# Performance work log

Measured on AMD Instinct MI355X. Metric: run time of the kernel, lower is better.

## Reference

```python
import jax, jax.numpy as jnp
import numpy as np
import math

EMBED_DIM = 128
NUM_HEADS = 8
HEAD_DIM = EMBED_DIM // NUM_HEADS
# Faithful to the source's concat bug: heads [0,1,1,2,3,4,5,6] (head 7 dropped, head 1 duplicated)
HEAD_ORDER = [0, 1, 1, 2, 3, 4, 5, 6]


def setup_inputs() -> dict:
    key = jax.random.key(0)
    ks = jax.random.split(key, 7)
    B, S = 4, 2048
    input_embeddings = jax.random.normal(ks[0], (B, S, EMBED_DIM), dtype=jnp.float32)
    token_attention_masks = jax.random.randint(ks[1], (B, S), 0, 2, dtype=jnp.int64)
    # torch.rand -> uniform [0,1)
    w_query = jax.random.uniform(ks[2], (EMBED_DIM, EMBED_DIM), dtype=jnp.float32)
    w_key = jax.random.uniform(ks[3], (EMBED_DIM, EMBED_DIM), dtype=jnp.float32)
    w_value = jax.random.uniform(ks[4], (EMBED_DIM, EMBED_DIM), dtype=jnp.float32)
    # nn.Linear params
    lim = 1.0 / math.sqrt(EMBED_DIM)
    lin_w = jax.random.uniform(ks[5], (EMBED_DIM, EMBED_DIM), dtype=jnp.float32, minval=-lim, maxval=lim)
    lin_b = jax.random.uniform(ks[6], (EMBED_DIM,), dtype=jnp.float32, minval=-lim, maxval=lim)
    return {"input_embeddings": input_embeddings, "token_attention_masks": token_attention_masks,
            "w_query": w_query, "w_key": w_key, "w_value": w_value, "lin_w": lin_w, "lin_b": lin_b}


def reference(input_embeddings, token_attention_masks, w_query, w_key, w_value, lin_w, lin_b):
    B, S, _ = input_embeddings.shape
    q = input_embeddings @ w_query  # [B,S,D]
    k = input_embeddings @ w_key
    v = input_embeddings @ w_value
    # split heads: [B,S,H,hd] -> [B,H,S,hd]
    qh = q.reshape(B, S, NUM_HEADS, HEAD_DIM).transpose(0, 2, 1, 3)
    kh = k.reshape(B, S, NUM_HEADS, HEAD_DIM).transpose(0, 2, 1, 3)
    vh = v.reshape(B, S, NUM_HEADS, HEAD_DIM).transpose(0, 2, 1, 3)
    # NOTE: source scales by sqrt(full embedding dim), not sqrt(head_dim)
    scale = 1.0 / math.sqrt(EMBED_DIM)
    scores = jnp.einsum('bhsd,bhtd->bhst', qh, kh) * scale  # [B,H,S,S]
    # mask: 0 -> -1000, 1 -> 0; broadcast over query positions
    mask = jnp.where(token_attention_masks == 0, -1000.0, 0.0).astype(scores.dtype)  # [B,S]
    scores = scores + mask[:, None, None, :]
    probs = jax.nn.softmax(scores, axis=-1)
    out_h = jnp.einsum('bhst,bhtd->bhsd', probs, vh)  # [B,H,S,hd]
    # buggy concat order kept faithful
    attn_out = jnp.concatenate([out_h[:, i] for i in HEAD_ORDER], axis=-1)  # [B,S,D]
    return attn_out @ lin_w.T + lin_b
```

## Files before the change

kernel.cpp:

```cpp
#include <hip/hip_runtime.h>
#include <stdint.h>

typedef unsigned short u16;
typedef unsigned int   u32;
typedef float   f32x4  __attribute__((ext_vector_type(4)));
typedef float   f32x16 __attribute__((ext_vector_type(16)));
typedef __bf16  bf16x8 __attribute__((ext_vector_type(8)));
typedef u32     u32x4  __attribute__((ext_vector_type(4)));
typedef u32     u32x2  __attribute__((ext_vector_type(2)));

union BF8 { bf16x8 v; u16 s[8]; u32x4 q; };

__device__ __forceinline__ u16 f2b_rne(float f) {
    u32 u = __builtin_bit_cast(u32, f);
    u32 r = u + 0x7FFFu + ((u >> 16) & 1u);
    return (u16)(r >> 16);
}
__device__ __forceinline__ u16 f2b_trunc(float f) {
    return (u16)(__builtin_bit_cast(u32, f) >> 16);
}
__device__ __forceinline__ float b2f(u16 h) {
    u32 u = ((u32)h) << 16;
    return __builtin_bit_cast(float, u);
}
__device__ __forceinline__ bf16x8 ld_bf8(const u16* p) {
    BF8 t; t.q = *(const u32x4*)p; return t.v;
}
__device__ __forceinline__ f32x16 zero16() {
    f32x16 z;
#pragma unroll
    for (int i = 0; i < 16; i++) z[i] = 0.f;
    return z;
}
__device__ __forceinline__ f32x4 zero4() {
    f32x4 z;
#pragma unroll
    for (int i = 0; i < 4; i++) z[i] = 0.f;
    return z;
}

#define SCALE2 0.1275312959479341f
#define MBIAS2 -1442.6950408889634f

__global__ __launch_bounds__(256) void proj_kernel(
    const float* __restrict__ x, const float* __restrict__ wq,
    const float* __restrict__ wk, const float* __restrict__ wv,
    u16* Qph, u16* Qpl, u16* Kph, u16* Kpl, u16* VT)
{
    int typ  = blockIdx.y;
    int ct   = threadIdx.x >> 6;
    int lane = threadIdx.x & 63;
    int m = lane & 31, kg = lane >> 5;
    int r0 = blockIdx.x * 32;
    int c = ct * 32 + m;

    const float* wp = (typ == 0) ? wq : (typ == 1) ? wk : wv;

    f32x16 acc = zero16();
#pragma unroll 4
    for (int kk = 0; kk < 128; kk += 16) {
        const float* xp = x + (size_t)(r0 + m) * 128 + kk + kg * 8;
        f32x4 x0 = *(const f32x4*)xp;
        f32x4 x1 = *(const f32x4*)(xp + 4);
        BF8 ah, al;
#pragma unroll
        for (int j = 0; j < 4; j++) {
            u16 hb = f2b_trunc(x0[j]);
            ah.s[j] = hb; al.s[j] = f2b_trunc(x0[j] - b2f(hb));
            u16 hb2 = f2b_trunc(x1[j]);
            ah.s[4 + j] = hb2; al.s[4 + j] = f2b_trunc(x1[j] - b2f(hb2));
        }
        const float* wcol = wp + (size_t)(kk + kg * 8) * 128 + c;
        if (typ < 2) {
            BF8 bh, bl_;
#pragma unroll
            for (int j = 0; j < 8; j++) {
                float w = wcol[(size_t)j * 128];
                u16 hb = f2b_trunc(w);
                bh.s[j] = hb; bl_.s[j] = f2b_trunc(w - b2f(hb));
            }
            acc = __builtin_amdgcn_mfma_f32_32x32x16_bf16(ah.v, bh.v, acc, 0, 0, 0);
            acc = __builtin_amdgcn_mfma_f32_32x32x16_bf16(ah.v, bl_.v, acc, 0, 0, 0);
            acc = __builtin_amdgcn_mfma_f32_32x32x16_bf16(al.v, bh.v, acc, 0, 0, 0);
        } else {
            BF8 bh;
#pragma unroll
            for (int j = 0; j < 8; j++) bh.s[j] = f2b_rne(wcol[(size_t)j * 128]);
            acc = __builtin_amdgcn_mfma_f32_32x32x16_bf16(ah.v, bh.v, acc, 0, 0, 0);
        }
    }

    int b = r0 >> 11, sl = r0 & 2047;
    if (typ < 2) {
        u16* H = typ ? Kph : Qph;
        u16* L = typ ? Kpl : Qpl;
        int hh = c >> 4, d = c & 15;
        if (hh == 7) return;
        float scl = (typ == 0) ? SCALE2 : 1.0f;
        size_t hb_off = (size_t)(b * 8 + hh) * 2048 * 16 + d;
#pragma unroll
        for (int r = 0; r < 16; r++) {
            int row = (r & 3) + 8 * (r >> 2) + 4 * kg;
            float v = acc[r] * scl;
            u16 hi = f2b_trunc(v);
            size_t idx = hb_off + (size_t)(sl + row) * 16;
            H[idx] = hi;
            L[idx] = f2b_trunc(v - b2f(hi));
        }
    } else {
        if ((c >> 4) == 7) return;
#pragma unroll
        for (int rg = 0; rg < 4; rg++) {
            int rowb = rg * 8 + 4 * kg;
            BF8 pk;
#pragma unroll
            for (int q = 0; q < 4; q++) pk.s[q] = f2b_rne(acc[rg * 4 + q]);
            u32x4 tmp = pk.q;
            *(u32*)(VT + (size_t)(b * 128 + c) * 2048 + sl + rowb)     = tmp[0];
            *(u32*)(VT + (size_t)(b * 128 + c) * 2048 + sl + rowb + 2) = tmp[1];
        }
    }
}

__global__ __launch_bounds__(256, 7) void attn_kernel(
    const u16* __restrict__ Qph, const u16* __restrict__ Qpl,
    const u16* __restrict__ Kph, const u16* __restrict__ Kpl,
    const u16* __restrict__ VT, const int* __restrict__ mask, u16* AO)
{
    __shared__ char smem[16896];
    u16*   pbuf  = (u16*)smem;
    float* biasC = (float*)(smem + 8192);
    float* lsmax = (float*)(smem + 16384);
    float* obuf  = (float*)smem;
    float* lbuf  = (float*)(smem + 8192);

    int bid = blockIdx.x;
    int bh = bid % 28;
    int qt = bid / 28;
    int b = bh / 7, h = bh % 7;
    int wave = threadIdx.x >> 6, lane = threadIdx.x & 63;
    int m = lane & 31, kg = lane >> 5;
    int qs = qt * 32;

    {
        int e0 = threadIdx.x * 8;
        const int* mp = mask + b * 2048;
        float v[8];
#pragma unroll
        for (int j = 0; j < 8; j++) {
            int e = e0 + j;
            int ti = e >> 5, kgg = (e >> 4) & 1, r = e & 15;
            int key = ti * 32 + (r & 3) + 8 * (r >> 2) + 4 * kgg;
            v[j] = (mp[key] != 0) ? 0.0f : MBIAS2;
        }
        *(f32x4*)(biasC + e0)     = *(const f32x4*)&v[0];
        *(f32x4*)(biasC + e0 + 4) = *(const f32x4*)&v[4];
    }
    __syncthreads();

    size_t headoff = (size_t)(b * 8 + h) * 2048 * 16;
    bf16x8 qfh = ld_bf8(Qph + headoff + (size_t)(qs + m) * 16 + kg * 8);
    bf16x8 qfl = ld_bf8(Qpl + headoff + (size_t)(qs + m) * 16 + kg * 8);
    const u16* kbh = Kph + headoff;
    const u16* kbl = Kpl + headoff;

    int t0 = wave * 512;

    float mloc = -3.0e38f;
    {
        bf16x8 khc = ld_bf8(kbh + (size_t)(t0 + m) * 16 + kg * 8);
        for (int t = t0; t < t0 + 512; t += 32) {
            int tn = (t + 32 < t0 + 512) ? (t + 32) : t0;
            bf16x8 khn = ld_bf8(kbh + (size_t)(tn + m) * 16 + kg * 8);
            f32x16 ci = *(const f32x16*)(biasC + (t >> 5) * 32 + kg * 16);
            f32x16 sc = __builtin_amdgcn_mfma_f32_32x32x16_bf16(khc, qfh, ci, 0, 0, 0);
#pragma unroll
            for (int r = 0; r < 16; r++) mloc = fmaxf(mloc, sc[r]);
            khc = khn;
        }
    }
    mloc = fmaxf(mloc, __shfl_xor(mloc, 32, 64));
    if (kg == 0) lsmax[m * 4 + wave] = mloc;
    __syncthreads();
    f32x4 mv = *(const f32x4*)(lsmax + m * 4);
    float mrow = fmaxf(fmaxf(mv[0], mv[1]), fmaxf(mv[2], mv[3]));

    f32x4 o0 = zero4(), o1 = zero4(), l0 = zero4(), l1 = zero4();
    BF8 onesu;
#pragma unroll
    for (int j = 0; j < 8; j++) onesu.s[j] = 0x3F80;
    bf16x8 ones = onesu.v;

    int q16 = lane & 15, krow = lane >> 4;
    const u16* vtb = VT + (size_t)(b * 128 + h * 16 + q16) * 2048;
    int msw = (m >> 1) & 3;
    int qsw = (q16 >> 1) & 3;
    u16* pwb = pbuf + wave * 1024 + m * 32 + kg * 4;
    const u16* pr0 = pbuf + wave * 1024 + q16 * 32 + ((krow ^ qsw) * 8);
    const u16* pr1 = pr0 + 16 * 32;

    bf16x8 khc = ld_bf8(kbh + (size_t)(t0 + m) * 16 + kg * 8);
    bf16x8 klc = ld_bf8(kbl + (size_t)(t0 + m) * 16 + kg * 8);

    for (int t = t0; t < t0 + 512; t += 32) {
        int tn = (t + 32 < t0 + 512) ? (t + 32) : t0;
        bf16x8 khn = ld_bf8(kbh + (size_t)(tn + m) * 16 + kg * 8);
        bf16x8 kln = ld_bf8(kbl + (size_t)(tn + m) * 16 + kg * 8);
        bf16x8 vf  = ld_bf8(vtb + t + krow * 8);

        f32x16 sc = *(const f32x16*)(biasC + (t >> 5) * 32 + kg * 16);
        sc = __builtin_amdgcn_mfma_f32_32x32x16_bf16(khc, qfl, sc, 0, 0, 0);
        sc = __builtin_amdgcn_mfma_f32_32x32x16_bf16(klc, qfh, sc, 0, 0, 0);
        sc = __builtin_amdgcn_mfma_f32_32x32x16_bf16(khc, qfh, sc, 0, 0, 0);
#pragma unroll
        for (int rg = 0; rg < 4; rg++) {
            float e0 = __builtin_amdgcn_exp2f(sc[rg * 4 + 0] - mrow);
            float e1 = __builtin_amdgcn_exp2f(sc[rg * 4 + 1] - mrow);
            float e2 = __builtin_amdgcn_exp2f(sc[rg * 4 + 2] - mrow);
            float e3 = __builtin_amdgcn_exp2f(sc[rg * 4 + 3] - mrow);
            u32x2 pk;
            pk[0] = __builtin_amdgcn_perm(__builtin_bit_cast(u32, e1),
                                          __builtin_bit_cast(u32, e0), 0x07060302u);
            pk[1] = __builtin_amdgcn_perm(__builtin_bit_cast(u32, e3),
                                          __builtin_bit_cast(u32, e2), 0x07060302u);
            *(u32x2*)(pwb + ((rg ^ msw) * 8)) = pk;
        }
        bf16x8 p0 = *(const bf16x8*)pr0;
        bf16x8 p1 = *(const bf16x8*)pr1;
        o0 = __builtin_amdgcn_mfma_f32_16x16x32_bf16(p0, vf, o0, 0, 0, 0);
        o1 = __builtin_amdgcn_mfma_f32_16x16x32_bf16(p1, vf, o1, 0, 0, 0);
        l0 = __builtin_amdgcn_mfma_f32_16x16x32_bf16(p0, ones, l0, 0, 0, 0);
        l1 = __builtin_amdgcn_mfma_f32_16x16x32_bf16(p1, ones, l1, 0, 0, 0);
        khc = khn; klc = kln;
    }

    __syncthreads();

    *(f32x4*)(obuf + wave * 512 + q16 * 32 + krow * 4)      = o0;
    *(f32x4*)(obuf + wave * 512 + q16 * 32 + krow * 4 + 16) = o1;
    if (q16 == 0) {
        *(f32x4*)(lbuf + wave * 32 + krow * 4)      = l0;
        *(f32x4*)(lbuf + wave * 32 + krow * 4 + 16) = l1;
    }
    __syncthreads();

    int dd = threadIdx.x & 15, q = threadIdx.x >> 4;
    int slot0 = (h == 0) ? 0 : h + 1;
#pragma unroll
    for (int hf = 0; hf < 2; hf++) {
        int qq = q + hf * 16;
        float os = obuf[0 * 512 + dd * 32 + qq] + obuf[1 * 512 + dd * 32 + qq]
                 + obuf[2 * 512 + dd * 32 + qq] + obuf[3 * 512 + dd * 32 + qq];
        float ls = lbuf[0 * 32 + qq] + lbuf[1 * 32 + qq]
                 + lbuf[2 * 32 + qq] + lbuf[3 * 32 + qq];
        u16 vb = f2b_rne(os * __builtin_amdgcn_rcpf(ls));
        int orow = b * 2048 + qs + qq;
        AO[orow * 128 + slot0 * 16 + dd] = vb;
        if (h == 1) AO[orow * 128 + 16 + dd] = vb;
    }
}

__global__ __launch_bounds__(256) void fin_kernel(
    const u16* __restrict__ AO, const float* __restrict__ lw,
    const float* __restrict__ lb, float* out)
{
    int ct   = threadIdx.x >> 6;
    int lane = threadIdx.x & 63;
    int m = lane & 31, kg = lane >> 5;
    int r0 = blockIdx.x * 32;
    int c = ct * 32 + m;

    f32x16 acc = zero16();
#pragma unroll 4
    for (int kk = 0; kk < 128; kk += 16) {
        bf16x8 af = ld_bf8(AO + (size_t)(r0 + m) * 128 + kk + kg * 8);
        const float* wp = lw + (size_t)c * 128 + kk + kg * 8;
        f32x4 w0 = *(const f32x4*)wp;
        f32x4 w1 = *(const f32x4*)(wp + 4);
        BF8 bfr;
#pragma unroll
        for (int j = 0; j < 4; j++) {
            bfr.s[j]     = f2b_rne(w0[j]);
            bfr.s[4 + j] = f2b_rne(w1[j]);
        }
        acc = __builtin_amdgcn_mfma_f32_32x32x16_bf16(af, bfr.v, acc, 0, 0, 0);
    }
    float bias = lb[c];
#pragma unroll
    for (int r = 0; r < 16; r++) {
        int row = (r & 3) + 8 * (r >> 2) + 4 * kg;
        out[(size_t)(r0 + row) * 128 + c] = acc[r] + bias;
    }
}

extern "C" void kernel_launch(void* const* d_in, const int* in_sizes, int n_in,
                              void* d_out, int out_size, void* d_ws, size_t ws_size,
                              hipStream_t stream)
{
    const float* x    = (const float*)d_in[0];
    const int*   mask = (const int*)d_in[1];
    const float* wq   = (const float*)d_in[2];
    const float* wk   = (const float*)d_in[3];
    const float* wv   = (const float*)d_in[4];
    const float* lw   = (const float*)d_in[5];
    const float* lb   = (const float*)d_in[6];
    float* out = (float*)d_out;

    char* ws = (char*)d_ws;
    u16* Qph = (u16*)(ws + 0 * 2097152);
    u16* Qpl = (u16*)(ws + 1 * 2097152);
    u16* Kph = (u16*)(ws + 2 * 2097152);
    u16* Kpl = (u16*)(ws + 3 * 2097152);
    u16* VT  = (u16*)(ws + 4 * 2097152);
    u16* AO  = (u16*)(ws + 5 * 2097152);

    proj_kernel<<<dim3(256, 3), 256, 0, stream>>>(x, wq, wk, wv,
                                                  Qph, Qpl, Kph, Kpl, VT);
    attn_kernel<<<1792, 256, 0, stream>>>(Qph, Qpl, Kph, Kpl, VT, mask, AO);
    fin_kernel<<<256, 256, 0, stream>>>(AO, lw, lb, out);
}
```

Before: 123.4 us.

## Compact unmasked keys and values so attention skips masked positions

```diff
diff --git a/kernel.cpp b/kernel.cpp
--- a/kernel.cpp
+++ b/kernel.cpp
@@ -40,11 +40,61 @@
 }
 
 #define SCALE2 0.1275312959479341f
-#define MBIAS2 -1442.6950408889634f
+
+__global__ __launch_bounds__(256) void prep_kernel(
+    const int* __restrict__ mask, int* __restrict__ pos,
+    int* __restrict__ Lout, u16* Kph, u16* Kpl, u16* VT)
+{
+    int b = blockIdx.x >> 3, slice = blockIdx.x & 7;
+    const int* mp = mask + b * 2048;
+    __shared__ int Lsh;
+    int tid = threadIdx.x;
+    if (tid < 64) {
+        int base = tid * 32;
+        int mv[32]; int c = 0;
+#pragma unroll
+        for (int j = 0; j < 32; j++) { mv[j] = mp[base + j]; c += (mv[j] != 0); }
+        int off = c;
+#pragma unroll
+        for (int d = 1; d < 64; d <<= 1) {
+            int o = __shfl_up(off, d, 64);
+            if (tid >= d) off += o;
+        }
+        if (slice == 0) {
+            int p = off - c;
+#pragma unroll
+            for (int j = 0; j < 32; j++) {
+                pos[b * 2048 + base + j] = mv[j] ? p : -1;
+                p += (mv[j] != 0);
+            }
+            if (tid == 63) Lout[b] = off;
+        }
+        if (tid == 63) Lsh = off;
+    }
+    __syncthreads();
+    int L = Lsh;
+    int npad = (L + 127) & ~127; if (npad < 128) npad = 128;
+    int padn = npad - L;
+    if (padn > 0) {
+        int e0 = slice * 2048;
+        for (int e = e0 + tid; e < e0 + 2048; e += 256) {
+            int d = e & 15, k = (e >> 4) & 127, h = e >> 11;
+            if (k < padn) {
+                size_t o = ((size_t)(b * 8 + h) * 2048 + (L + k)) * 16 + d;
+                Kph[o] = 0; Kpl[o] = 0;
+            }
+        }
+        for (int e = e0 + tid; e < e0 + 2048; e += 256) {
+            int k = e & 127, cc = e >> 7;
+            if (k < padn) VT[(size_t)(b * 128 + cc) * 2048 + (L + k)] = 0;
+        }
+    }
+}
 
 __global__ __launch_bounds__(256) void proj_kernel(
     const float* __restrict__ x, const float* __restrict__ wq,
     const float* __restrict__ wk, const float* __restrict__ wv,
+    const int* __restrict__ pos,
     u16* Qph, u16* Qpl, u16* Kph, u16* Kpl, u16* VT)
 {
     int typ  = blockIdx.y;
@@ -91,33 +141,44 @@
     }
 
     int b = r0 >> 11, sl = r0 & 2047;
-    if (typ < 2) {
-        u16* H = typ ? Kph : Qph;
-        u16* L = typ ? Kpl : Qpl;
-        int hh = c >> 4, d = c & 15;
-        if (hh == 7) return;
-        float scl = (typ == 0) ? SCALE2 : 1.0f;
+    int hh = c >> 4, d = c & 15;
+    if (hh == 7) return;
+    if (typ == 0) {
         size_t hb_off = (size_t)(b * 8 + hh) * 2048 * 16 + d;
 #pragma unroll
         for (int r = 0; r < 16; r++) {
             int row = (r & 3) + 8 * (r >> 2) + 4 * kg;
-            float v = acc[r] * scl;
+            float v = acc[r] * SCALE2;
             u16 hi = f2b_trunc(v);
             size_t idx = hb_off + (size_t)(sl + row) * 16;
-            H[idx] = hi;
-            L[idx] = f2b_trunc(v - b2f(hi));
+            Qph[idx] = hi;
+            Qpl[idx] = f2b_trunc(v - b2f(hi));
+        }
+    } else if (typ == 1) {
+        const int* pb = pos + b * 2048;
+        size_t hb_off = (size_t)(b * 8 + hh) * 2048 * 16 + d;
+#pragma unroll
+        for (int r = 0; r < 16; r++) {
+            int row = (r & 3) + 8 * (r >> 2) + 4 * kg;
+            int p = pb[sl + row];
+            if (p < 0) continue;
+            float v = acc[r];
+            u16 hi = f2b_trunc(v);
+            size_t idx = hb_off + (size_t)p * 16;
+            Kph[idx] = hi;
+            Kpl[idx] = f2b_trunc(v - b2f(hi));
         }
     } else {
-        if ((c >> 4) == 7) return;
+        const int* pb = pos + b * 2048;
 #pragma unroll
         for (int rg = 0; rg < 4; rg++) {
-            int rowb = rg * 8 + 4 * kg;
-            BF8 pk;
-#pragma unroll
-            for (int q = 0; q < 4; q++) pk.s[q] = f2b_rne(acc[rg * 4 + q]);
-            u32x4 tmp = pk.q;
-            *(u32*)(VT + (size_t)(b * 128 + c) * 2048 + sl + rowb)     = tmp[0];
-            *(u32*)(VT + (size_t)(b * 128 + c) * 2048 + sl + rowb + 2) = tmp[1];
+#pragma unroll
+            for (int q = 0; q < 4; q++) {
+                int row = rg * 8 + 4 * kg + q;
+                int p = pb[sl + row];
+                if (p >= 0)
+                    VT[(size_t)(b * 128 + c) * 2048 + p] = f2b_rne(acc[rg * 4 + q]);
+            }
         }
     }
 }
@@ -125,14 +186,13 @@
 __global__ __launch_bounds__(256, 7) void attn_kernel(
     const u16* __restrict__ Qph, const u16* __restrict__ Qpl,
     const u16* __restrict__ Kph, const u16* __restrict__ Kpl,
-    const u16* __restrict__ VT, const int* __restrict__ mask, u16* AO)
-{
-    __shared__ char smem[16896];
+    const u16* __restrict__ VT, const int* __restrict__ Larr, u16* AO)
+{
+    __shared__ char smem[9216];
     u16*   pbuf  = (u16*)smem;
-    float* biasC = (float*)(smem + 8192);
-    float* lsmax = (float*)(smem + 16384);
     float* obuf  = (float*)smem;
     float* lbuf  = (float*)(smem + 8192);
+    float* lsmax = (float*)(smem + 8704);
 
     int bid = blockIdx.x;
     int bh = bid % 28;
@@ -142,21 +202,10 @@
     int m = lane & 31, kg = lane >> 5;
     int qs = qt * 32;
 
-    {
-        int e0 = threadIdx.x * 8;
-        const int* mp = mask + b * 2048;
-        float v[8];
-#pragma unroll
-        for (int j = 0; j < 8; j++) {
-            int e = e0 + j;
-            int ti = e >> 5, kgg = (e >> 4) & 1, r = e & 15;
-            int key = ti * 32 + (r & 3) + 8 * (r >> 2) + 4 * kgg;
-            v[j] = (mp[key] != 0) ? 0.0f : MBIAS2;
-        }
-        *(f32x4*)(biasC + e0)     = *(const f32x4*)&v[0];
-        *(f32x4*)(biasC + e0 + 4) = *(const f32x4*)&v[4];
-    }
-    __syncthreads();
+    int L = Larr[b];
+    int npad = (L + 127) & ~127; if (npad < 128) npad = 128;
+    int kpw = npad >> 2;
+    int t0 = wave * kpw, tend = t0 + kpw;
 
     size_t headoff = (size_t)(b * 8 + h) * 2048 * 16;
     bf16x8 qfh = ld_bf8(Qph + headoff + (size_t)(qs + m) * 16 + kg * 8);
@@ -164,18 +213,23 @@
     const u16* kbh = Kph + headoff;
     const u16* kbl = Kpl + headoff;
 
-    int t0 = wave * 512;
-
     float mloc = -3.0e38f;
     {
         bf16x8 khc = ld_bf8(kbh + (size_t)(t0 + m) * 16 + kg * 8);
-        for (int t = t0; t < t0 + 512; t += 32) {
-            int tn = (t + 32 < t0 + 512) ? (t + 32) : t0;
+        for (int t = t0; t < tend; t += 32) {
+            int tn = (t + 32 < tend) ? (t + 32) : t0;
             bf16x8 khn = ld_bf8(kbh + (size_t)(tn + m) * 16 + kg * 8);
-            f32x16 ci = *(const f32x16*)(biasC + (t >> 5) * 32 + kg * 16);
-            f32x16 sc = __builtin_amdgcn_mfma_f32_32x32x16_bf16(khc, qfh, ci, 0, 0, 0);
-#pragma unroll
-            for (int r = 0; r < 16; r++) mloc = fmaxf(mloc, sc[r]);
+            f32x16 sc = __builtin_amdgcn_mfma_f32_32x32x16_bf16(khc, qfh, zero16(), 0, 0, 0);
+            if (t + 32 <= L) {
+#pragma unroll
+                for (int r = 0; r < 16; r++) mloc = fmaxf(mloc, sc[r]);
+            } else {
+#pragma unroll
+                for (int r = 0; r < 16; r++) {
+                    int key = t + (r & 3) + 8 * (r >> 2) + 4 * kg;
+                    if (key < L) mloc = fmaxf(mloc, sc[r]);
+                }
+            }
             khc = khn;
         }
     }
@@ -202,22 +256,30 @@
     bf16x8 khc = ld_bf8(kbh + (size_t)(t0 + m) * 16 + kg * 8);
     bf16x8 klc = ld_bf8(kbl + (size_t)(t0 + m) * 16 + kg * 8);
 
-    for (int t = t0; t < t0 + 512; t += 32) {
-        int tn = (t + 32 < t0 + 512) ? (t + 32) : t0;
+    for (int t = t0; t < tend; t += 32) {
+        int tn = (t + 32 < tend) ? (t + 32) : t0;
         bf16x8 khn = ld_bf8(kbh + (size_t)(tn + m) * 16 + kg * 8);
         bf16x8 kln = ld_bf8(kbl + (size_t)(tn + m) * 16 + kg * 8);
         bf16x8 vf  = ld_bf8(vtb + t + krow * 8);
 
-        f32x16 sc = *(const f32x16*)(biasC + (t >> 5) * 32 + kg * 16);
+        f32x16 sc = zero16();
         sc = __builtin_amdgcn_mfma_f32_32x32x16_bf16(khc, qfl, sc, 0, 0, 0);
         sc = __builtin_amdgcn_mfma_f32_32x32x16_bf16(klc, qfh, sc, 0, 0, 0);
         sc = __builtin_amdgcn_mfma_f32_32x32x16_bf16(khc, qfh, sc, 0, 0, 0);
+        bool tail = (t + 32 > L);
 #pragma unroll
         for (int rg = 0; rg < 4; rg++) {
             float e0 = __builtin_amdgcn_exp2f(sc[rg * 4 + 0] - mrow);
             float e1 = __builtin_amdgcn_exp2f(sc[rg * 4 + 1] - mrow);
             float e2 = __builtin_amdgcn_exp2f(sc[rg * 4 + 2] - mrow);
             float e3 = __builtin_amdgcn_exp2f(sc[rg * 4 + 3] - mrow);
+            if (tail) {
+                int kb = t + rg * 8 + kg * 4;
+                e0 = (kb + 0 < L) ? e0 : 0.f;
+                e1 = (kb + 1 < L) ? e1 : 0.f;
+                e2 = (kb + 2 < L) ? e2 : 0.f;
+                e3 = (kb + 3 < L) ? e3 : 0.f;
+            }
             u32x2 pk;
             pk[0] = __builtin_amdgcn_perm(__builtin_bit_cast(u32, e1),
                                           __builtin_bit_cast(u32, e0), 0x07060302u);
@@ -313,9 +375,12 @@
     u16* Kpl = (u16*)(ws + 3 * 2097152);
     u16* VT  = (u16*)(ws + 4 * 2097152);
     u16* AO  = (u16*)(ws + 5 * 2097152);
-
-    proj_kernel<<<dim3(256, 3), 256, 0, stream>>>(x, wq, wk, wv,
+    int* pos  = (int*)(ws + 6 * 2097152);
+    int* Larr = (int*)(ws + 6 * 2097152 + 65536);
+
+    prep_kernel<<<32, 256, 0, stream>>>(mask, pos, Larr, Kph, Kpl, VT);
+    proj_kernel<<<dim3(256, 3), 256, 0, stream>>>(x, wq, wk, wv, pos,
                                                   Qph, Qpl, Kph, Kpl, VT);
-    attn_kernel<<<1792, 256, 0, stream>>>(Qph, Qpl, Kph, Kpl, VT, mask, AO);
+    attn_kernel<<<1792, 256, 0, stream>>>(Qph, Qpl, Kph, Kpl, VT, Larr, AO);
     fin_kernel<<<256, 256, 0, stream>>>(AO, lw, lb, out);
 }
```

Measured after the change: 122.7 us. No clear change (-0.6%).
